# Kernel optimization log

Measured on AMD Instinct MI355X. Metric: run time of the kernel, lower is better.

## Reference

```python
import jax, jax.numpy as jnp
import numpy as np

N, E, B = 50000, 1600000, 64
RAW, EMB, HID = 32, 128, 128
NH, HD = 8, 16  # heads, head_dim (HID = NH*HD)
LH, A, O = 128, 7, 2


def setup_inputs():
    key = jax.random.key(0)
    ks = iter(jax.random.split(key, 48))
    def p(shape, s=0.05):
        return (jax.random.normal(next(ks), shape, dtype=jnp.float32) * s)
    inp = {}
    inp['node_features'] = jax.random.normal(next(ks), (N, RAW), dtype=jnp.float32)
    inp['edge_index'] = jax.random.randint(next(ks), (2, E), 0, N)
    inp['batch'] = jnp.sort(jax.random.randint(next(ks), (N,), 0, B))
    inp['w'] = jax.random.uniform(next(ks), (B, O), dtype=jnp.float32)
    inp['h_prev'] = jnp.zeros((B, LH), jnp.float32)
    inp['c_prev'] = jnp.zeros((B, LH), jnp.float32)
    inp['W_emb'] = p((EMB, RAW)); inp['b_emb'] = jnp.zeros((EMB,), jnp.float32)
    inp['W_g1'] = p((HID, EMB)); inp['b_g1'] = jnp.zeros((HID,), jnp.float32)
    inp['W_g2'] = p((HID, HID)); inp['b_g2'] = jnp.zeros((HID,), jnp.float32)
    inp['Wq'] = p((HID, HID)); inp['bq'] = jnp.zeros((HID,), jnp.float32)
    inp['Wk'] = p((HID, HID)); inp['bk'] = jnp.zeros((HID,), jnp.float32)
    inp['Wv'] = p((HID, HID)); inp['bv'] = jnp.zeros((HID,), jnp.float32)
    inp['Wskip'] = p((HID, HID)); inp['bskip'] = jnp.zeros((HID,), jnp.float32)
    inp['W_gam'] = p((HID, O)); inp['b_gam'] = jnp.zeros((HID,), jnp.float32)
    inp['W_bet'] = p((HID, O)); inp['b_bet'] = jnp.zeros((HID,), jnp.float32)
    inp['W_ih'] = p((4 * LH, HID)); inp['b_ih'] = jnp.zeros((4 * LH,), jnp.float32)
    inp['W_hh'] = p((4 * LH, LH)); inp['b_hh'] = jnp.zeros((4 * LH,), jnp.float32)
    inp['ln_g'] = jnp.ones((LH,), jnp.float32); inp['ln_b'] = jnp.zeros((LH,), jnp.float32)
    inp['W_a1'] = p((LH, LH)); inp['b_a1'] = jnp.zeros((LH,), jnp.float32)
    inp['W_a2'] = p((A * O, LH)); inp['b_a2'] = jnp.zeros((A * O,), jnp.float32)
    inp['W_v1'] = p((LH, LH)); inp['b_v1'] = jnp.zeros((LH,), jnp.float32)
    inp['W_v2'] = p((O, LH)); inp['b_v2'] = jnp.zeros((O,), jnp.float32)
    return inp


def reference(node_features, edge_index, batch, w, h_prev, c_prev,
              W_emb, b_emb, W_g1, b_g1, W_g2, b_g2,
              Wq, bq, Wk, bk, Wv, bv, Wskip, bskip,
              W_gam, b_gam, W_bet, b_bet,
              W_ih, W_hh, b_ih, b_hh, ln_g, ln_b,
              W_a1, b_a1, W_a2, b_a2, W_v1, b_v1, W_v2, b_v2):
    n = node_features.shape[0]
    src, dst = edge_index[0], edge_index[1]
    # GCN with self-loops and symmetric normalization (PyG gcn_norm)
    loop = jnp.arange(n)
    srcl = jnp.concatenate([src, loop])
    dstl = jnp.concatenate([dst, loop])
    deg = jax.ops.segment_sum(jnp.ones_like(dstl, jnp.float32), dstl, n)
    dinv = jnp.where(deg > 0, jax.lax.rsqrt(jnp.maximum(deg, 1.0)), 0.0)
    norm = dinv[srcl] * dinv[dstl]

    def gcn(x, W, b):
        xw = x @ W.T
        return jax.ops.segment_sum(norm[:, None] * xw[srcl], dstl, n) + b

    x = jax.nn.relu(node_features @ W_emb.T + b_emb)
    x = jax.nn.relu(gcn(x, W_g1, b_g1))
    # dropout(p=0.2) is identity in eval mode
    x = jax.nn.relu(gcn(x, W_g2, b_g2))

    # TransformerConv (no self-loops, concat heads, root skip)
    q = (x @ Wq.T + bq).reshape(n, NH, HD)
    k = (x @ Wk.T + bk).reshape(n, NH, HD)
    v = (x @ Wv.T + bv).reshape(n, NH, HD)
    logits = jnp.sum(q[dst] * k[src], axis=-1) / np.sqrt(HD)  # [E, NH]
    m = jax.ops.segment_max(logits, dst, n)
    m = jnp.where(jnp.isfinite(m), m, 0.0)
    ex = jnp.exp(logits - m[dst])
    den = jax.ops.segment_sum(ex, dst, n)
    alpha = ex / jnp.maximum(den[dst], 1e-16)
    agg = jax.ops.segment_sum(alpha[..., None] * v[src], dst, n).reshape(n, NH * HD)
    x = agg + x @ Wskip.T + bskip

    # FiLM conditioning on objective weights
    g = (w @ W_gam.T + b_gam)[batch]
    bb = (w @ W_bet.T + b_bet)[batch]
    x = x * (1.0 + g) + bb

    # global mean pool per graph
    bsz = h_prev.shape[0]
    s = jax.ops.segment_sum(x, batch, bsz)
    cnt = jax.ops.segment_sum(jnp.ones((n,), jnp.float32), batch, bsz)
    ge = s / jnp.maximum(cnt, 1.0)[:, None]

    # LSTM cell (torch gate order i, f, g, o)
    gates = ge @ W_ih.T + b_ih + h_prev @ W_hh.T + b_hh
    i, f, gc, o = jnp.split(gates, 4, axis=-1)
    i = jax.nn.sigmoid(i); f = jax.nn.sigmoid(f)
    gc = jnp.tanh(gc); o = jax.nn.sigmoid(o)
    c_raw = f * c_prev + i * gc
    h_raw = o * jnp.tanh(c_raw)  # h computed before c is clamped (as in source)
    c_new = jnp.clip(c_raw, -1e6, 1e6)

    # LayerNorm on h
    mu = jnp.mean(h_raw, axis=-1, keepdims=True)
    var = jnp.var(h_raw, axis=-1, keepdims=True)
    h_new = (h_raw - mu) * jax.lax.rsqrt(var + 1e-5) * ln_g + ln_b
    # lstm dropout is identity in eval mode

    val = jax.nn.relu(h_new @ W_v1.T + b_v1) @ W_v2.T + b_v2  # [B, O]
    adv = (jax.nn.relu(h_new @ W_a1.T + b_a1) @ W_a2.T + b_a2).reshape(bsz, A, O)
    qv = val[:, None, :] + (adv - jnp.mean(adv, axis=1, keepdims=True))
    qv = jnp.nan_to_num(qv, nan=0.0, posinf=1e6, neginf=-1e6)
    qv = jnp.clip(qv, -100.0, 100.0)
    return qv, h_new, c_new
```

## Files before the change

kernel.cpp:

```cpp
#include <hip/hip_runtime.h>
#include <hip/hip_bf16.h>
#include <math.h>

typedef unsigned int uint;
typedef unsigned short ushort_t;
typedef __bf16 bf16_t;
typedef bf16_t bf16x8 __attribute__((ext_vector_type(8)));
typedef float f32x4 __attribute__((ext_vector_type(4)));
typedef float f32x2 __attribute__((ext_vector_type(2)));

__device__ inline float2 bf2_unpack(uint u) {
    union { uint i; float f; } a, b;
    a.i = u << 16;
    b.i = u & 0xffff0000u;
    return make_float2(a.f, b.f);
}

__device__ inline uint bf2_pack(float lo, float hi) {
    __hip_bfloat162 h;
    h.x = __float2bfloat16(lo);
    h.y = __float2bfloat16(hi);
    return *(uint*)&h;
}

template<bool WORD>
__device__ __forceinline__ float2 fp8x2_unpack(uint u) {
    f32x2 r = __builtin_amdgcn_cvt_pk_f32_fp8((int)u, WORD);
    return make_float2(r[0], r[1]);
}
__device__ __forceinline__ int fp8x2_pack(float a, float b) {
    return __builtin_amdgcn_cvt_pk_fp8_f32(a, b, 0, false);
}

__device__ inline void store_out(float* p, float v) { *p = v; }
__device__ inline void store_out(__hip_bfloat16* p, float v) { *p = __float2bfloat16(v); }

#define RFL(x) __builtin_amdgcn_readfirstlane(x)

#define SCL_XW 32.f
#define SCL_KV 16.f
#define BK_SH 5
#define CHUNK 16384

__global__ __launch_bounds__(1024) void k_bcount(const int* __restrict__ ei, int* __restrict__ bcnt,
                                                 int E, int nbk) {
    __shared__ int hist[2048];
    int t = threadIdx.x;
    for (int i = t; i < nbk; i += 1024) hist[i] = 0;
    __syncthreads();
    int e0 = blockIdx.x * CHUNK;
    int e1 = e0 + CHUNK; if (e1 > E) e1 = E;
    for (int e = e0 + t; e < e1; e += 1024)
        atomicAdd(&hist[(uint)ei[E + e] >> BK_SH], 1);
    __syncthreads();
    for (int i = t; i < nbk; i += 1024) {
        int c = hist[i];
        if (c) atomicAdd(&bcnt[i], c);
    }
}

__global__ __launch_bounds__(1024) void k_bscan(const int* __restrict__ bcnt, int* __restrict__ boff, int nbk) {
    __shared__ int tmp[1024];
    int t = threadIdx.x;
    int per = (nbk + 1023) >> 10;
    int s0 = t * per, s1 = s0 + per; if (s1 > nbk) s1 = nbk;
    int sum = 0;
    for (int i = s0; i < s1; ++i) sum += bcnt[i];
    tmp[t] = sum;
    __syncthreads();
    for (int d = 1; d < 1024; d <<= 1) {
        int a = (t >= d) ? tmp[t - d] : 0;
        __syncthreads();
        tmp[t] += a;
        __syncthreads();
    }
    int carry = tmp[t] - sum;
    for (int i = s0; i < s1; ++i) { boff[i] = carry; carry += bcnt[i]; }
    if (t == 1023) boff[nbk] = tmp[1023];
}

__global__ __launch_bounds__(1024) void k_bfill(const int* __restrict__ ei, const int* __restrict__ boff,
                                                int* __restrict__ bcur, uint2* __restrict__ pairs,
                                                int E, int nbk) {
    __shared__ int hist[2048];
    __shared__ int basep[2048];
    int t = threadIdx.x;
    for (int i = t; i < nbk; i += 1024) hist[i] = 0;
    __syncthreads();
    int e0 = blockIdx.x * CHUNK;
    int e1 = e0 + CHUNK; if (e1 > E) e1 = E;
    for (int e = e0 + t; e < e1; e += 1024)
        atomicAdd(&hist[(uint)ei[E + e] >> BK_SH], 1);
    __syncthreads();
    for (int i = t; i < nbk; i += 1024) {
        int c = hist[i];
        basep[i] = c ? atomicAdd(&bcur[i], c) : 0;
        hist[i] = 0;
    }
    __syncthreads();
    for (int e = e0 + t; e < e1; e += 1024) {
        int d = ei[E + e];
        int s = ei[e];
        int b = (uint)d >> BK_SH;
        int p = atomicAdd(&hist[b], 1);
        pairs[boff[b] + basep[b] + p] = make_uint2((uint)d, (uint)s);
    }
}

__global__ __launch_bounds__(256) void k_bucket(const uint2* __restrict__ pairs, const int* __restrict__ boff,
                                                int* __restrict__ off, float* __restrict__ dinv,
                                                int* __restrict__ col, int N, int nbk, int E) {
    int b = blockIdx.x, t = threadIdx.x;
    __shared__ int cnt[32], excl[32], cur[32];
    int base = boff[b], end = boff[b + 1];
    if (t < 32) cnt[t] = 0;
    __syncthreads();
    for (int i = base + t; i < end; i += 256) {
        uint2 p = pairs[i];
        atomicAdd(&cnt[p.x & 31], 1);
    }
    __syncthreads();
    if (t == 0) {
        int run = base;
        #pragma unroll
        for (int j = 0; j < 32; ++j) { excl[j] = run; cur[j] = run; run += cnt[j]; }
    }
    __syncthreads();
    if (t < 32) {
        int node = (b << BK_SH) + t;
        if (node < N) {
            off[node] = excl[t];
            dinv[node] = rsqrtf((float)(cnt[t] + 1));
        }
    }
    if (b == nbk - 1 && t == 0) off[N] = E;
    for (int i = base + t; i < end; i += 256) {
        uint2 p = pairs[i];
        int pos = atomicAdd(&cur[p.x & 31], 1);
        col[pos] = (int)p.y;
    }
}

__global__ __launch_bounds__(256) void k_cvt6(const float* __restrict__ s0, const float* __restrict__ s1,
                                              const float* __restrict__ s2, const float* __restrict__ s3,
                                              const float* __restrict__ s4, const float* __restrict__ s5,
                                              __hip_bfloat16* __restrict__ dst) {
    int i = blockIdx.x * 256 + threadIdx.x;
    if (i >= 6 * 16384) return;
    int m = i >> 14;
    const float* s = (m == 0) ? s0 : (m == 1) ? s1 : (m == 2) ? s2 : (m == 3) ? s3 : (m == 4) ? s4 : s5;
    dst[i] = __float2bfloat16(s[i & 16383]);
}

template<int FI, bool BIAS, bool RELU, typename OUT>
__global__ __launch_bounds__(256) void k_linear(const float* __restrict__ x, const float* __restrict__ W,
                                                const float* __restrict__ b, OUT* __restrict__ y, int n) {
    __shared__ float4 Wt4[(FI / 4) * 128];
    __shared__ float4 xl[2][FI / 4];
    int t = threadIdx.x & 127;
    int h = threadIdx.x >> 7;
    {
        const float4* Wrow = (const float4*)(W + (size_t)t * FI);
        #pragma unroll
        for (int k4 = h * (FI / 8); k4 < (h + 1) * (FI / 8); ++k4) Wt4[k4 * 128 + t] = Wrow[k4];
    }
    float bias = 0.f;
    if (BIAS) bias = b[t];
    __syncthreads();
    for (int n0 = blockIdx.x * 2; n0 < n; n0 += gridDim.x * 2) {
        int nn = n0 + h;
        if (nn < n && t < FI / 4) xl[h][t] = ((const float4*)(x + (size_t)nn * FI))[t];
        __syncthreads();
        if (nn < n) {
            float acc = bias;
            #pragma unroll
            for (int k4 = 0; k4 < FI / 4; ++k4) {
                float4 xv = xl[h][k4];
                float4 wv = Wt4[k4 * 128 + t];
                acc += xv.x * wv.x + xv.y * wv.y + xv.z * wv.z + xv.w * wv.w;
            }
            if (RELU) acc = fmaxf(acc, 0.f);
            store_out(&y[(size_t)nn * 128 + t], acc);
        }
        __syncthreads();
    }
}

__global__ __launch_bounds__(256) void k_lin_mfma_scale(const __hip_bfloat16* __restrict__ X,
                                                        const __hip_bfloat16* __restrict__ W,
                                                        const float* __restrict__ dinv,
                                                        ushort_t* __restrict__ XW8, int n) {
    int wave = threadIdx.x >> 6, lane = threadIdx.x & 63;
    int r0 = blockIdx.x * 64 + wave * 16;
    if (r0 >= n) return;
    int mrow = r0 + (lane & 15);
    if (mrow >= n) mrow = n - 1;
    int kk4 = lane >> 4;
    const bf16x8* xr = (const bf16x8*)((const bf16_t*)X + (size_t)mrow * 128);
    bf16x8 a0 = xr[0 * 4 + kk4];
    bf16x8 a1 = xr[1 * 4 + kk4];
    bf16x8 a2 = xr[2 * 4 + kk4];
    bf16x8 a3 = xr[3 * 4 + kk4];
    int orow = (lane >> 4) * 4;
    int ocol = lane & 15;
    float dv[4];
    #pragma unroll
    for (int j = 0; j < 4; ++j) {
        int row = r0 + orow + j;
        dv[j] = ((row < n) ? dinv[row] : 0.f) * SCL_XW;
    }
    #pragma unroll
    for (int c = 0; c < 8; ++c) {
        const bf16x8* wr = (const bf16x8*)((const bf16_t*)W + (size_t)(c * 16 + (lane & 15)) * 128);
        bf16x8 b0 = wr[0 * 4 + kk4];
        bf16x8 b1 = wr[1 * 4 + kk4];
        bf16x8 b2 = wr[2 * 4 + kk4];
        bf16x8 b3 = wr[3 * 4 + kk4];
        f32x4 acc = {0.f, 0.f, 0.f, 0.f};
        acc = __builtin_amdgcn_mfma_f32_16x16x32_bf16(a0, b0, acc, 0, 0, 0);
        acc = __builtin_amdgcn_mfma_f32_16x16x32_bf16(a1, b1, acc, 0, 0, 0);
        acc = __builtin_amdgcn_mfma_f32_16x16x32_bf16(a2, b2, acc, 0, 0, 0);
        acc = __builtin_amdgcn_mfma_f32_16x16x32_bf16(a3, b3, acc, 0, 0, 0);
        int gcol = c * 16 + ocol;
        #pragma unroll
        for (int j = 0; j < 4; ++j) {
            int row = r0 + orow + j;
            float v = acc[j] * dv[j];
            float vnb = __shfl_down(v, 1);
            if (((lane & 1) == 0) && row < n) {
                int pk = fp8x2_pack(v, vnb);
                XW8[(size_t)row * 64 + (gcol >> 1)] = (ushort_t)(pk & 0xffff);
            }
        }
    }
}

__global__ __launch_bounds__(256) void k_qkvs_mfma(const __hip_bfloat16* __restrict__ X,
                                                   const __hip_bfloat16* __restrict__ W4,
                                                   const float* __restrict__ bq, const float* __restrict__ bk,
                                                   const float* __restrict__ bv, const float* __restrict__ bs,
                                                   __hip_bfloat16* __restrict__ Cqb, uint* __restrict__ KV8,
                                                   __hip_bfloat16* __restrict__ Bb, int n) {
    int wave = threadIdx.x >> 6, lane = threadIdx.x & 63;
    int r0 = blockIdx.x * 64 + wave * 16;
    if (r0 >= n) return;
    int mrow = r0 + (lane & 15);
    if (mrow >= n) mrow = n - 1;
    int kk4 = lane >> 4;
    const bf16x8* xr = (const bf16x8*)((const bf16_t*)X + (size_t)mrow * 128);
    bf16x8 a0 = xr[0 * 4 + kk4];
    bf16x8 a1 = xr[1 * 4 + kk4];
    bf16x8 a2 = xr[2 * 4 + kk4];
    bf16x8 a3 = xr[3 * 4 + kk4];
    int orow = (lane >> 4) * 4;
    int ocol = lane & 15;
    float karr[32];
    #pragma unroll
    for (int m = 0; m < 4; ++m) {
        const bf16_t* Wm = (const bf16_t*)W4 + (size_t)m * 16384;
        const float* bias = (m == 0) ? bq : (m == 1) ? bk : (m == 2) ? bv : bs;
        #pragma unroll
        for (int c = 0; c < 8; ++c) {
            const bf16x8* wr = (const bf16x8*)(Wm + (size_t)(c * 16 + (lane & 15)) * 128);
            bf16x8 b0 = wr[0 * 4 + kk4];
            bf16x8 b1 = wr[1 * 4 + kk4];
            bf16x8 b2 = wr[2 * 4 + kk4];
            bf16x8 b3 = wr[3 * 4 + kk4];
            f32x4 acc = {0.f, 0.f, 0.f, 0.f};
            acc = __builtin_amdgcn_mfma_f32_16x16x32_bf16(a0, b0, acc, 0, 0, 0);
            acc = __builtin_amdgcn_mfma_f32_16x16x32_bf16(a1, b1, acc, 0, 0, 0);
            acc = __builtin_amdgcn_mfma_f32_16x16x32_bf16(a2, b2, acc, 0, 0, 0);
            acc = __builtin_amdgcn_mfma_f32_16x16x32_bf16(a3, b3, acc, 0, 0, 0);
            int gcol = c * 16 + ocol;
            float bb = bias[gcol];
            #pragma unroll
            for (int j = 0; j < 4; ++j) {
                int row = r0 + orow + j;
                float v = acc[j] + bb;
                if (m == 1) karr[c * 4 + j] = v * SCL_KV;
                if (m == 0) {
                    if (row < n) store_out(&Cqb[(size_t)row * 128 + gcol], v * (0.25f / SCL_KV));
                } else if (m == 2) {
                    int pk = fp8x2_pack(karr[c * 4 + j], v * SCL_KV);
                    int nb = __shfl_down(pk, 1);
                    if (((lane & 1) == 0) && row < n) {
                        uint u = (uint)(pk & 0xffff) | ((uint)nb << 16);
                        KV8[(size_t)row * 64 + (gcol >> 1)] = u;
                    }
                } else if (m == 3) {
                    if (row < n) store_out(&Bb[(size_t)row * 128 + gcol], v);
                }
            }
        }
    }
}

__device__ __forceinline__ void gcn_load8(const int* __restrict__ col, int i, const ushort_t* __restrict__ xw,
                                          int lane, uint (&u)[8]) {
    #pragma unroll
    for (int j = 0; j < 8; ++j) {
        int c = RFL(col[i + j]);
        u[j] = (uint)xw[(size_t)c * 64 + lane];
    }
}

__device__ __forceinline__ void gcn_proc8(const uint (&u)[8], float2& acc) {
    float sx = 0.f, sy = 0.f;
    #pragma unroll
    for (int j = 0; j < 8; ++j) {
        float2 x = fp8x2_unpack<false>(u[j]);
        sx += x.x;
        sy += x.y;
    }
    acc.x += sx;
    acc.y += sy;
}

__global__ __launch_bounds__(256) void k_gcn_agg(const ushort_t* __restrict__ xw, const int* __restrict__ off,
                                                 const int* __restrict__ col, const float* __restrict__ dinv,
                                                 const float* __restrict__ bias, __hip_bfloat162* __restrict__ y, int n) {
    int wid = RFL((int)((blockIdx.x * 256 + threadIdx.x) >> 6));
    int lane = threadIdx.x & 63;
    if (wid >= n) return;
    float di = dinv[wid] * (1.f / SCL_XW);
    float2 acc = fp8x2_unpack<false>((uint)xw[(size_t)wid * 64 + lane]);
    int i = RFL(off[wid]), i1 = RFL(off[wid + 1]);
    uint ua[8], ub[8];
    if (i + 8 <= i1) {
        gcn_load8(col, i, xw, lane, ua);
        while (true) {
            int inext = i + 8;
            bool more = (inext + 8 <= i1);
            if (more) gcn_load8(col, inext, xw, lane, ub);
            gcn_proc8(ua, acc);
            i = inext;
            if (!more) break;
            inext = i + 8;
            more = (inext + 8 <= i1);
            if (more) gcn_load8(col, inext, xw, lane, ua);
            gcn_proc8(ub, acc);
            i = inext;
            if (!more) break;
        }
    }
    for (; i < i1; ++i) {
        int c0 = RFL(col[i]);
        float2 x0 = fp8x2_unpack<false>((uint)xw[(size_t)c0 * 64 + lane]);
        acc.x += x0.x;
        acc.y += x0.y;
    }
    float2 b2 = ((const float2*)bias)[lane];
    __hip_bfloat162 o;
    o.x = __float2bfloat16(fmaxf(di * acc.x + b2.x, 0.f));
    o.y = __float2bfloat16(fmaxf(di * acc.y + b2.y, 0.f));
    y[(size_t)wid * 64 + lane] = o;
}

__device__ __forceinline__ void attn_load8(const int* __restrict__ col, int i, const uint* __restrict__ kv8,
                                           int lane, uint (&u)[8]) {
    #pragma unroll
    for (int j = 0; j < 8; ++j) {
        int c = RFL(col[i + j]);
        u[j] = kv8[((size_t)c << 6) + lane];
    }
}

__device__ __forceinline__ void attn_proc8(const uint (&u)[8], float2 q2,
                                           float& m, float& s, float2& acc) {
    float l[8];
    #pragma unroll
    for (int j = 0; j < 8; ++j) {
        float2 p0 = fp8x2_unpack<false>(u[j]);
        float2 p1 = fp8x2_unpack<true>(u[j]);
        l[j] = q2.x * p0.x + q2.y * p1.x;
    }
    #pragma unroll
    for (int j = 0; j < 8; ++j) l[j] += __shfl_xor(l[j], 1);
    #pragma unroll
    for (int j = 0; j < 8; ++j) l[j] += __shfl_xor(l[j], 2);
    #pragma unroll
    for (int j = 0; j < 8; ++j) l[j] += __shfl_xor(l[j], 4);
    float mx = fmaxf(fmaxf(fmaxf(l[0], l[1]), fmaxf(l[2], l[3])), fmaxf(fmaxf(l[4], l[5]), fmaxf(l[6], l[7])));
    if (mx > m) {
        float corr = __expf(m - mx);
        s *= corr;
        acc.x *= corr;
        acc.y *= corr;
        m = mx;
    }
    float sx = 0.f, sy = 0.f, ss = 0.f;
    #pragma unroll
    for (int j = 0; j < 8; ++j) {
        float e = __expf(l[j] - m);
        float2 p0 = fp8x2_unpack<false>(u[j]);
        float2 p1 = fp8x2_unpack<true>(u[j]);
        ss += e;
        sx += e * p0.y;
        sy += e * p1.y;
    }
    s += ss;
    acc.x += sx;
    acc.y += sy;
}

__global__ __launch_bounds__(256) void k_attn(const uint* __restrict__ qb, const uint* __restrict__ kv8,
                                              const int* __restrict__ off, const int* __restrict__ col,
                                              uint* __restrict__ io, int n) {
    int wid = RFL((int)((blockIdx.x * 256 + threadIdx.x) >> 6));
    int lane = threadIdx.x & 63;
    if (wid >= n) return;
    float2 q2 = bf2_unpack(qb[(size_t)wid * 64 + lane]);
    float m = -INFINITY, s = 0.f;
    float2 acc = make_float2(0.f, 0.f);
    int i = RFL(off[wid]), i1 = RFL(off[wid + 1]);
    uint ua[8], ub[8];
    if (i + 8 <= i1) {
        attn_load8(col, i, kv8, lane, ua);
        while (true) {
            int inext = i + 8;
            bool more = (inext + 8 <= i1);
            if (more) attn_load8(col, inext, kv8, lane, ub);
            attn_proc8(ua, q2, m, s, acc);
            i = inext;
            if (!more) break;
            inext = i + 8;
            more = (inext + 8 <= i1);
            if (more) attn_load8(col, inext, kv8, lane, ua);
            attn_proc8(ub, q2, m, s, acc);
            i = inext;
            if (!more) break;
        }
    }
    for (; i < i1; ++i) {
        int c0 = RFL(col[i]);
        uint u0 = kv8[((size_t)c0 << 6) + lane];
        float2 p0 = fp8x2_unpack<false>(u0);
        float2 p1 = fp8x2_unpack<true>(u0);
        float l0 = q2.x * p0.x + q2.y * p1.x;
        l0 += __shfl_xor(l0, 1);
        l0 += __shfl_xor(l0, 2);
        l0 += __shfl_xor(l0, 4);
        if (l0 > m) {
            float corr = __expf(m - l0);
            s *= corr;
            acc.x *= corr;
            acc.y *= corr;
            m = l0;
        }
        float e0 = __expf(l0 - m);
        s += e0;
        acc.x += e0 * p0.y;
        acc.y += e0 * p1.y;
    }
    float inv = (1.f / SCL_KV) / fmaxf(s, 1e-16f);
    uint* orow = io + (size_t)wid * 64 + lane;
    float2 o2 = bf2_unpack(*orow);
    o2.x += acc.x * inv;
    o2.y += acc.y * inv;
    *orow = bf2_pack(o2.x, o2.y);
}

__global__ __launch_bounds__(128) void k_pool(const __hip_bfloat16* __restrict__ x, const int* __restrict__ batch,
                                              float* __restrict__ gsum, float* __restrict__ cnt, int n) {
    int t = threadIdx.x;
    int start = blockIdx.x * 64;
    int end = start + 64; if (end > n) end = n;
    if (start >= n) return;
    int cur = batch[start];
    float acc = 0.f;
    int run = 0;
    for (int nn = start; nn < end; ++nn) {
        int g = batch[nn];
        if (g != cur) {
            atomicAdd(&gsum[cur * 128 + t], acc);
            if (t == 0) atomicAdd(&cnt[cur], (float)run);
            acc = 0.f; run = 0; cur = g;
        }
        acc += __bfloat162float(x[(size_t)nn * 128 + t]);
        run++;
    }
    atomicAdd(&gsum[cur * 128 + t], acc);
    if (t == 0) atomicAdd(&cnt[cur], (float)run);
}

__global__ __launch_bounds__(128) void k_final(
    const float* __restrict__ gsum, const float* __restrict__ cnt, const float* __restrict__ w,
    const float* __restrict__ Wgam, const float* __restrict__ bgam,
    const float* __restrict__ Wbet, const float* __restrict__ bbet,
    const float* __restrict__ hprev, const float* __restrict__ cprev,
    const float* __restrict__ Wih, const float* __restrict__ bih,
    const float* __restrict__ Whh, const float* __restrict__ bhh,
    const float* __restrict__ lng, const float* __restrict__ lnb,
    const float* __restrict__ Wa1, const float* __restrict__ ba1,
    const float* __restrict__ Wa2, const float* __restrict__ ba2,
    const float* __restrict__ Wv1, const float* __restrict__ bv1,
    const float* __restrict__ Wv2, const float* __restrict__ bv2,
    float* __restrict__ out_qv, float* __restrict__ out_h, float* __restrict__ out_c) {
    int g = blockIdx.x, t = threadIdx.x;
    __shared__ __align__(16) float ge[128], hp[128], hn[128], r1[128], a1s[128], red[128];
    __shared__ float adv[16], val[2], mu_s, var_s;

    float w0 = w[g * 2 + 0], w1 = w[g * 2 + 1];
    float c = fmaxf(cnt[g], 1.f);
    float mn = gsum[g * 128 + t] / c;
    float gam = w0 * Wgam[2 * t] + w1 * Wgam[2 * t + 1] + bgam[t];
    float bet = w0 * Wbet[2 * t] + w1 * Wbet[2 * t + 1] + bbet[t];
    ge[t] = (1.f + gam) * mn + bet;
    hp[t] = hprev[g * 128 + t];
    __syncthreads();

    float gi = bih[t] + bhh[t];
    float gf = bih[128 + t] + bhh[128 + t];
    float gg = bih[256 + t] + bhh[256 + t];
    float go = bih[384 + t] + bhh[384 + t];
    {
        const float4* ge4 = (const float4*)ge;
        const float4* hp4 = (const float4*)hp;
        const float4* Ai = (const float4*)(Wih + (size_t)t * 128);
        const float4* Af = (const float4*)(Wih + (size_t)(128 + t) * 128);
        const float4* Ag = (const float4*)(Wih + (size_t)(256 + t) * 128);
        const float4* Ao = (const float4*)(Wih + (size_t)(384 + t) * 128);
        const float4* Hi = (const float4*)(Whh + (size_t)t * 128);
        const float4* Hf = (const float4*)(Whh + (size_t)(128 + t) * 128);
        const float4* Hg = (const float4*)(Whh + (size_t)(256 + t) * 128);
        const float4* Ho = (const float4*)(Whh + (size_t)(384 + t) * 128);
        #pragma unroll 4
        for (int k4 = 0; k4 < 32; ++k4) {
            float4 a = ge4[k4], h4 = hp4[k4], u;
            u = Ai[k4]; gi += a.x * u.x + a.y * u.y + a.z * u.z + a.w * u.w;
            u = Hi[k4]; gi += h4.x * u.x + h4.y * u.y + h4.z * u.z + h4.w * u.w;
            u = Af[k4]; gf += a.x * u.x + a.y * u.y + a.z * u.z + a.w * u.w;
            u = Hf[k4]; gf += h4.x * u.x + h4.y * u.y + h4.z * u.z + h4.w * u.w;
            u = Ag[k4]; gg += a.x * u.x + a.y * u.y + a.z * u.z + a.w * u.w;
            u = Hg[k4]; gg += h4.x * u.x + h4.y * u.y + h4.z * u.z + h4.w * u.w;
            u = Ao[k4]; go += a.x * u.x + a.y * u.y + a.z * u.z + a.w * u.w;
            u = Ho[k4]; go += h4.x * u.x + h4.y * u.y + h4.z * u.z + h4.w * u.w;
        }
    }
    float ig = 1.f / (1.f + __expf(-gi));
    float fg = 1.f / (1.f + __expf(-gf));
    float gc = tanhf(gg);
    float og = 1.f / (1.f + __expf(-go));
    float craw = fg * cprev[g * 128 + t] + ig * gc;
    float hraw = og * tanhf(craw);
    out_c[g * 128 + t] = fminf(fmaxf(craw, -1e6f), 1e6f);

    red[t] = hraw;
    __syncthreads();
    for (int s2 = 64; s2 > 0; s2 >>= 1) { if (t < s2) red[t] += red[t + s2]; __syncthreads(); }
    if (t == 0) mu_s = red[0] * (1.f / 128.f);
    __syncthreads();
    float mu = mu_s;
    float d = hraw - mu;
    red[t] = d * d;
    __syncthreads();
    for (int s2 = 64; s2 > 0; s2 >>= 1) { if (t < s2) red[t] += red[t + s2]; __syncthreads(); }
    if (t == 0) var_s = red[0] * (1.f / 128.f);
    __syncthreads();
    float hv = d * rsqrtf(var_s + 1e-5f) * lng[t] + lnb[t];
    hn[t] = hv;
    out_h[g * 128 + t] = hv;
    __syncthreads();

    float accv = bv1[t], acca = ba1[t];
    {
        const float4* hn4 = (const float4*)hn;
        const float4* V1 = (const float4*)(Wv1 + (size_t)t * 128);
        const float4* A1 = (const float4*)(Wa1 + (size_t)t * 128);
        #pragma unroll 4
        for (int k4 = 0; k4 < 32; ++k4) {
            float4 hh = hn4[k4], u;
            u = V1[k4]; accv += hh.x * u.x + hh.y * u.y + hh.z * u.z + hh.w * u.w;
            u = A1[k4]; acca += hh.x * u.x + hh.y * u.y + hh.z * u.z + hh.w * u.w;
        }
    }
    r1[t] = fmaxf(accv, 0.f);
    a1s[t] = fmaxf(acca, 0.f);
    __syncthreads();
    if (t < 2) {
        float s = bv2[t];
        const float4* V2 = (const float4*)(Wv2 + (size_t)t * 128);
        const float4* r4 = (const float4*)r1;
        for (int k4 = 0; k4 < 32; ++k4) { float4 u = V2[k4], rr = r4[k4]; s += rr.x * u.x + rr.y * u.y + rr.z * u.z + rr.w * u.w; }
        val[t] = s;
    }
    if (t < 14) {
        float s = ba2[t];
        const float4* A2 = (const float4*)(Wa2 + (size_t)t * 128);
        const float4* a4 = (const float4*)a1s;
        for (int k4 = 0; k4 < 32; ++k4) { float4 u = A2[k4], aa = a4[k4]; s += aa.x * u.x + aa.y * u.y + aa.z * u.z + aa.w * u.w; }
        adv[t] = s;
    }
    __syncthreads();
    if (t < 14) {
        int o = t & 1;
        float mo = (adv[o] + adv[o + 2] + adv[o + 4] + adv[o + 6] + adv[o + 8] + adv[o + 10] + adv[o + 12]) * (1.f / 7.f);
        float qq = val[o] + adv[t] - mo;
        if (isnan(qq)) qq = 0.f;
        qq = fminf(fmaxf(qq, -100.f), 100.f);
        out_qv[g * 14 + t] = qq;
    }
}

extern "C" void kernel_launch(void* const* d_in, const int* in_sizes, int n_in,
                              void* d_out, int out_size, void* d_ws, size_t ws_size,
                              hipStream_t stream) {
    const float* nf    = (const float*)d_in[0];
    const int*   ei    = (const int*)d_in[1];
    const int*   batch = (const int*)d_in[2];
    const float* w     = (const float*)d_in[3];
    const float* hprev = (const float*)d_in[4];
    const float* cprev = (const float*)d_in[5];
    const float* W_emb = (const float*)d_in[6];  const float* b_emb = (const float*)d_in[7];
    const float* W_g1  = (const float*)d_in[8];  const float* b_g1  = (const float*)d_in[9];
    const float* W_g2  = (const float*)d_in[10]; const float* b_g2  = (const float*)d_in[11];
    const float* Wq    = (const float*)d_in[12]; const float* bq    = (const float*)d_in[13];
    const float* Wk    = (const float*)d_in[14]; const float* bk    = (const float*)d_in[15];
    const float* Wv    = (const float*)d_in[16]; const float* bv    = (const float*)d_in[17];
    const float* Wskip = (const float*)d_in[18]; const float* bskip = (const float*)d_in[19];
    const float* Wgam  = (const float*)d_in[20]; const float* bgam  = (const float*)d_in[21];
    const float* Wbet  = (const float*)d_in[22]; const float* bbet  = (const float*)d_in[23];
    const float* Wih   = (const float*)d_in[24]; const float* bih   = (const float*)d_in[25];
    const float* Whh   = (const float*)d_in[26]; const float* bhh   = (const float*)d_in[27];
    const float* lng   = (const float*)d_in[28]; const float* lnb   = (const float*)d_in[29];
    const float* Wa1   = (const float*)d_in[30]; const float* ba1   = (const float*)d_in[31];
    const float* Wa2   = (const float*)d_in[32]; const float* ba2   = (const float*)d_in[33];
    const float* Wv1   = (const float*)d_in[34]; const float* bv1   = (const float*)d_in[35];
    const float* Wv2   = (const float*)d_in[36]; const float* bv2   = (const float*)d_in[37];

    int N = in_sizes[2];
    int E = in_sizes[1] / 2;
    int B = in_sizes[4] / 128;
    int nbk = (N + 31) >> BK_SH;

    char* p = (char*)d_ws;
    auto alloc = [&](size_t bytes) { char* r = p; p += (bytes + 511) & ~(size_t)511; return r; };
    int*   bcnt   = (int*)alloc((size_t)nbk * 4);
    int*   bcur   = (int*)alloc((size_t)nbk * 4);
    float* gsum   = (float*)alloc((size_t)B * 128 * 4);
    float* cnt    = (float*)alloc((size_t)B * 4);
    size_t zbytes = (size_t)(p - (char*)d_ws);
    int*   boff   = (int*)alloc((size_t)(nbk + 1) * 4);
    uint2* pairs  = (uint2*)alloc((size_t)E * 8);
    int*   off    = (int*)alloc((size_t)(N + 1) * 4);
    int*   col    = (int*)alloc((size_t)E * 4);
    float* dinv   = (float*)alloc((size_t)N * 4);
    __hip_bfloat16* Wc  = (__hip_bfloat16*)alloc((size_t)6 * 16384 * 2);
    __hip_bfloat16* X0b = (__hip_bfloat16*)alloc((size_t)N * 128 * 2);
    __hip_bfloat16* X1b = (__hip_bfloat16*)alloc((size_t)N * 128 * 2);
    ushort_t* XW8 = (ushort_t*)alloc((size_t)N * 128);
    uint*  KV8 = (uint*)alloc((size_t)N * 256);
    __hip_bfloat16* Cqb = (__hip_bfloat16*)alloc((size_t)N * 128 * 2);
    __hip_bfloat16* Bb  = (__hip_bfloat16*)alloc((size_t)N * 128 * 2);
    if ((size_t)(p - (char*)d_ws) > ws_size) return;

    (void)hipMemsetAsync(d_ws, 0, zbytes, stream);

    const __hip_bfloat16* Wg1b  = Wc + 0 * 16384;
    const __hip_bfloat16* Wg2b  = Wc + 1 * 16384;
    const __hip_bfloat16* Wqkvs = Wc + 2 * 16384;
    k_cvt6<<<384, 256, 0, stream>>>(W_g1, W_g2, Wq, Wk, Wv, Wskip, Wc);

    int gC = (E + CHUNK - 1) / CHUNK;
    k_bcount<<<gC, 1024, 0, stream>>>(ei, bcnt, E, nbk);
    k_bscan<<<1, 1024, 0, stream>>>(bcnt, boff, nbk);
    k_bfill<<<gC, 1024, 0, stream>>>(ei, boff, bcur, pairs, E, nbk);
    k_bucket<<<nbk, 256, 0, stream>>>(pairs, boff, off, dinv, col, N, nbk, E);

    int gN = (N + 3) / 4;
    int gM = (N + 63) / 64;

    k_linear<32, true, true, __hip_bfloat16><<<2048, 256, 0, stream>>>(nf, W_emb, b_emb, X0b, N);
    k_lin_mfma_scale<<<gM, 256, 0, stream>>>(X0b, Wg1b, dinv, XW8, N);
    k_gcn_agg<<<gN, 256, 0, stream>>>(XW8, off, col, dinv, b_g1, (__hip_bfloat162*)X1b, N);
    k_lin_mfma_scale<<<gM, 256, 0, stream>>>(X1b, Wg2b, dinv, XW8, N);
    k_gcn_agg<<<gN, 256, 0, stream>>>(XW8, off, col, dinv, b_g2, (__hip_bfloat162*)X0b, N);

    k_qkvs_mfma<<<gM, 256, 0, stream>>>(X0b, Wqkvs, bq, bk, bv, bskip, Cqb, KV8, Bb, N);
    k_attn<<<gN, 256, 0, stream>>>((const uint*)Cqb, KV8, off, col, (uint*)Bb, N);

    k_pool<<<gM, 128, 0, stream>>>(Bb, batch, gsum, cnt, N);

    float* out_qv = (float*)d_out;
    float* out_h  = out_qv + (size_t)B * 14;
    float* out_c  = out_h + (size_t)B * 128;
    k_final<<<B, 128, 0, stream>>>(gsum, cnt, w, Wgam, bgam, Wbet, bbet, hprev, cprev,
                                   Wih, bih, Whh, bhh, lng, lnb,
                                   Wa1, ba1, Wa2, ba2, Wv1, bv1, Wv2, bv2,
                                   out_qv, out_h, out_c);
}
```

Measured before the change: 374.7 us.

## Split K/V into separate fp8 halves and map attention lanes to edges

The packed KV8 row is relaid out so each 32-bit word holds two K values in its low half and two V values in its high half. The attention kernel now assigns each 8-lane group to one head, with each lane handling a different edge. Each lane loads 16 contiguous bytes of K/V per edge and computes the full 16-wide dot product itself, which removes the per-edge shuffle reductions and the scalar tail loop. The cost is 16 float accumulators per lane and a butterfly reduction across the 8 edge lanes at the end. Wavefronts with fewer than 8 remaining edges leave lanes idle and issue clamped duplicate loads.

```diff
diff --git a/kernel.cpp b/kernel.cpp
--- a/kernel.cpp
+++ b/kernel.cpp
@@ -281,10 +281,14 @@
                 if (m == 0) {
                     if (row < n) store_out(&Cqb[(size_t)row * 128 + gcol], v * (0.25f / SCL_KV));
                 } else if (m == 2) {
-                    int pk = fp8x2_pack(karr[c * 4 + j], v * SCL_KV);
-                    int nb = __shfl_down(pk, 1);
+                    float vv = v * SCL_KV;
+                    float kk = karr[c * 4 + j];
+                    float kn = __shfl_down(kk, 1);
+                    float vn = __shfl_down(vv, 1);
                     if (((lane & 1) == 0) && row < n) {
-                        uint u = (uint)(pk & 0xffff) | ((uint)nb << 16);
+                        int pkk = fp8x2_pack(kk, kn);
+                        int pkv = fp8x2_pack(vv, vn);
+                        uint u = ((uint)pkk & 0xffffu) | ((uint)pkv << 16);
                         KV8[(size_t)row * 64 + (gcol >> 1)] = u;
                     }
                 } else if (m == 3) {
@@ -356,51 +360,36 @@
     y[(size_t)wid * 64 + lane] = o;
 }
 
-__device__ __forceinline__ void attn_load8(const int* __restrict__ col, int i, const uint* __restrict__ kv8,
-                                           int lane, uint (&u)[8]) {
-    #pragma unroll
-    for (int j = 0; j < 8; ++j) {
-        int c = RFL(col[i + j]);
-        u[j] = kv8[((size_t)c << 6) + lane];
-    }
-}
-
-__device__ __forceinline__ void attn_proc8(const uint (&u)[8], float2 q2,
-                                           float& m, float& s, float2& acc) {
-    float l[8];
-    #pragma unroll
-    for (int j = 0; j < 8; ++j) {
-        float2 p0 = fp8x2_unpack<false>(u[j]);
-        float2 p1 = fp8x2_unpack<true>(u[j]);
-        l[j] = q2.x * p0.x + q2.y * p1.x;
-    }
-    #pragma unroll
-    for (int j = 0; j < 8; ++j) l[j] += __shfl_xor(l[j], 1);
-    #pragma unroll
-    for (int j = 0; j < 8; ++j) l[j] += __shfl_xor(l[j], 2);
-    #pragma unroll
-    for (int j = 0; j < 8; ++j) l[j] += __shfl_xor(l[j], 4);
-    float mx = fmaxf(fmaxf(fmaxf(l[0], l[1]), fmaxf(l[2], l[3])), fmaxf(fmaxf(l[4], l[5]), fmaxf(l[6], l[7])));
+__device__ __forceinline__ void attn_chunk(uint4 A, uint4 Bv, bool act, const float (&qf)[16],
+                                           float& m, float& s, float (&acc)[16]) {
+    uint au[8] = {A.x, A.y, A.z, A.w, Bv.x, Bv.y, Bv.z, Bv.w};
+    float l = 0.f;
+    #pragma unroll
+    for (int d = 0; d < 8; ++d) {
+        float2 kk = fp8x2_unpack<false>(au[d]);
+        l = fmaf(qf[2 * d], kk.x, l);
+        l = fmaf(qf[2 * d + 1], kk.y, l);
+    }
+    if (!act) l = -INFINITY;
+    float mx = l;
+    mx = fmaxf(mx, __shfl_xor(mx, 1));
+    mx = fmaxf(mx, __shfl_xor(mx, 2));
+    mx = fmaxf(mx, __shfl_xor(mx, 4));
     if (mx > m) {
         float corr = __expf(m - mx);
         s *= corr;
-        acc.x *= corr;
-        acc.y *= corr;
+        #pragma unroll
+        for (int f = 0; f < 16; ++f) acc[f] *= corr;
         m = mx;
     }
-    float sx = 0.f, sy = 0.f, ss = 0.f;
-    #pragma unroll
-    for (int j = 0; j < 8; ++j) {
-        float e = __expf(l[j] - m);
-        float2 p0 = fp8x2_unpack<false>(u[j]);
-        float2 p1 = fp8x2_unpack<true>(u[j]);
-        ss += e;
-        sx += e * p0.y;
-        sy += e * p1.y;
-    }
-    s += ss;
-    acc.x += sx;
-    acc.y += sy;
+    float e = act ? __expf(l - m) : 0.f;
+    s += e;
+    #pragma unroll
+    for (int d = 0; d < 8; ++d) {
+        float2 vv = fp8x2_unpack<true>(au[d]);
+        acc[2 * d] = fmaf(e, vv.x, acc[2 * d]);
+        acc[2 * d + 1] = fmaf(e, vv.y, acc[2 * d + 1]);
+    }
 }
 
 __global__ __launch_bounds__(256) void k_attn(const uint* __restrict__ qb, const uint* __restrict__ kv8,
@@ -408,55 +397,88 @@
                                               uint* __restrict__ io, int n) {
     int wid = RFL((int)((blockIdx.x * 256 + threadIdx.x) >> 6));
     int lane = threadIdx.x & 63;
+    int h = lane >> 3, j = lane & 7;
     if (wid >= n) return;
-    float2 q2 = bf2_unpack(qb[(size_t)wid * 64 + lane]);
+    float qf[16];
+    {
+        const uint4* q4 = (const uint4*)(qb + (size_t)wid * 64 + h * 8);
+        uint4 qa = q4[0], qc = q4[1];
+        uint qu[8] = {qa.x, qa.y, qa.z, qa.w, qc.x, qc.y, qc.z, qc.w};
+        #pragma unroll
+        for (int d = 0; d < 8; ++d) {
+            float2 t = bf2_unpack(qu[d]);
+            qf[2 * d] = t.x;
+            qf[2 * d + 1] = t.y;
+        }
+    }
+    float acc[16];
+    #pragma unroll
+    for (int f = 0; f < 16; ++f) acc[f] = 0.f;
     float m = -INFINITY, s = 0.f;
-    float2 acc = make_float2(0.f, 0.f);
     int i = RFL(off[wid]), i1 = RFL(off[wid + 1]);
-    uint ua[8], ub[8];
-    if (i + 8 <= i1) {
-        attn_load8(col, i, kv8, lane, ua);
+    uint4 A0, B0, A1, B1;
+    bool act0 = false, act1 = false;
+    if (i < i1) {
+        {
+            int idx = i + j; act0 = idx < i1;
+            int c = col[act0 ? idx : (i1 - 1)];
+            const uint4* pb = (const uint4*)(kv8 + ((size_t)(uint)c << 6) + (h << 3));
+            A0 = pb[0]; B0 = pb[1];
+        }
         while (true) {
             int inext = i + 8;
-            bool more = (inext + 8 <= i1);
-            if (more) attn_load8(col, inext, kv8, lane, ub);
-            attn_proc8(ua, q2, m, s, acc);
+            bool more = inext < i1;
+            if (more) {
+                int idx = inext + j; act1 = idx < i1;
+                int c = col[act1 ? idx : (i1 - 1)];
+                const uint4* pb = (const uint4*)(kv8 + ((size_t)(uint)c << 6) + (h << 3));
+                A1 = pb[0]; B1 = pb[1];
+            }
+            attn_chunk(A0, B0, act0, qf, m, s, acc);
             i = inext;
             if (!more) break;
             inext = i + 8;
-            more = (inext + 8 <= i1);
-            if (more) attn_load8(col, inext, kv8, lane, ua);
-            attn_proc8(ub, q2, m, s, acc);
+            more = inext < i1;
+            if (more) {
+                int idx = inext + j; act0 = idx < i1;
+                int c = col[act0 ? idx : (i1 - 1)];
+                const uint4* pb = (const uint4*)(kv8 + ((size_t)(uint)c << 6) + (h << 3));
+                A0 = pb[0]; B0 = pb[1];
+            }
+            attn_chunk(A1, B1, act1, qf, m, s, acc);
             i = inext;
             if (!more) break;
         }
     }
-    for (; i < i1; ++i) {
-        int c0 = RFL(col[i]);
-        uint u0 = kv8[((size_t)c0 << 6) + lane];
-        float2 p0 = fp8x2_unpack<false>(u0);
-        float2 p1 = fp8x2_unpack<true>(u0);
-        float l0 = q2.x * p0.x + q2.y * p1.x;
-        l0 += __shfl_xor(l0, 1);
-        l0 += __shfl_xor(l0, 2);
-        l0 += __shfl_xor(l0, 4);
-        if (l0 > m) {
-            float corr = __expf(m - l0);
-            s *= corr;
-            acc.x *= corr;
-            acc.y *= corr;
-            m = l0;
-        }
-        float e0 = __expf(l0 - m);
-        s += e0;
-        acc.x += e0 * p0.y;
-        acc.y += e0 * p1.y;
+    s += __shfl_xor(s, 1);
+    s += __shfl_xor(s, 2);
+    s += __shfl_xor(s, 4);
+    float r8[8];
+    #pragma unroll
+    for (int f = 0; f < 8; ++f) {
+        float send = (j & 4) ? acc[f] : acc[f + 8];
+        float recv = __shfl_xor(send, 4);
+        r8[f] = ((j & 4) ? acc[f + 8] : acc[f]) + recv;
+    }
+    float r4[4];
+    #pragma unroll
+    for (int f = 0; f < 4; ++f) {
+        float send = (j & 2) ? r8[f] : r8[f + 4];
+        float recv = __shfl_xor(send, 2);
+        r4[f] = ((j & 2) ? r8[f + 4] : r8[f]) + recv;
+    }
+    float r2[2];
+    #pragma unroll
+    for (int f = 0; f < 2; ++f) {
+        float send = (j & 1) ? r4[f] : r4[f + 2];
+        float recv = __shfl_xor(send, 1);
+        r2[f] = ((j & 1) ? r4[f + 2] : r4[f]) + recv;
     }
     float inv = (1.f / SCL_KV) / fmaxf(s, 1e-16f);
     uint* orow = io + (size_t)wid * 64 + lane;
     float2 o2 = bf2_unpack(*orow);
-    o2.x += acc.x * inv;
-    o2.y += acc.y * inv;
+    o2.x += r2[0] * inv;
+    o2.y += r2[1] * inv;
     *orow = bf2_pack(o2.x, o2.y);
 }
 
```

Measured after the change: 374.8 us. About the same (+0.0%).
